# Kernel optimization log

Measured on AMD Instinct MI355X. Metric: run time of the kernel, lower is better.

Reference implementation:

```python
import jax, jax.numpy as jnp
import numpy as np

B, C, Q, E, H = 8, 1024, 128, 512, 1024


def setup_inputs() -> dict:
    key = jax.random.key(0)
    ks = jax.random.split(key, 8)
    return {
        "context": jax.random.normal(ks[0], (B, C, E), jnp.float32),
        "question": jax.random.normal(ks[1], (B, Q, E), jnp.float32),
        "context_mask": jnp.ones((B, C), jnp.float32),
        "w_question": jax.random.normal(ks[2], (E,), jnp.float32),
        "w_context": jax.random.normal(ks[3], (E,), jnp.float32),
        "w_multiple": jax.random.normal(ks[4], (E,), jnp.float32),
        "W1": jax.random.normal(ks[5], (4 * E, H), jnp.float32) * 0.02,
        "b1": jnp.zeros((H,), jnp.float32),
        "W2": jax.random.normal(ks[6], (H, 4 * E), jnp.float32) * 0.02,
        "b2": jnp.zeros((4 * E,), jnp.float32),
    }


def reference(context, question, context_mask, w_question, w_context, w_multiple, W1, b1, W2, b2):
    # Dropout is identity at eval time.
    # Trilinear similarity: s[b,c,q] = q.w_q + ctx.w_c + sum_e q_e*ctx_e*w_m_e
    q_w = question @ w_question                                  # (B,Q)
    c_w = context @ w_context                                    # (B,C)
    mult = jnp.einsum("bqe,bce->bcq", question * w_multiple, context)  # avoids (B,C,Q,E)
    sim = q_w[:, None, :] + c_w[:, :, None] + mult               # (B,C,Q)

    # Context2Query: softmax over question dim (dim=2)
    c2q = jnp.einsum("bcq,bqe->bce", jax.nn.softmax(sim, axis=2), question)
    # Query2Context: max over question dim, softmax over context dim (dim=1)
    q2c = jnp.einsum("bc,bce->be", jax.nn.softmax(jnp.max(sim, axis=2), axis=1), context)  # (B,E)

    attended = jnp.concatenate(
        [context, c2q, context * c2q, context * q2c[:, None, :]], axis=2
    )  # (B,C,4E)

    # MaskedLinear: linear then zero out masked context positions
    m = context_mask[:, :, None]
    h = (attended @ W1 + b1) * m
    out = jax.nn.relu((h @ W2 + b2) * m)
    return out
```

## Files before the change

kernel.cpp:

```cpp
#include <hip/hip_runtime.h>

typedef __bf16 bf16;
typedef __bf16 bf16x2 __attribute__((ext_vector_type(2)));
typedef __bf16 bf16x4 __attribute__((ext_vector_type(4)));
typedef __bf16 bf16x8 __attribute__((ext_vector_type(8)));
typedef float f32x4 __attribute__((ext_vector_type(4)));

#define AS1 __attribute__((address_space(1)))
#define AS3 __attribute__((address_space(3)))

__device__ __forceinline__ void async_copy16(const void* g, void* l) {
  __builtin_amdgcn_global_load_lds((const AS1 void*)g, (AS3 void*)l, 16, 0, 0);
}

#define BB 8
#define CC 1024
#define QQ 128
#define EE 512
#define HH 1024
#define FOURE 2048

__global__ __launch_bounds__(256) void prep_kernel(
    const float* __restrict__ W1, const float* __restrict__ W2,
    const float* __restrict__ qst, const float* __restrict__ wmul,
    const float* __restrict__ wqv, bf16* __restrict__ W1T,
    bf16* __restrict__ W2T, bf16* __restrict__ qT,
    bf16* __restrict__ qmh, bf16* __restrict__ qml, float* __restrict__ qw) {
  __shared__ float tile[32][33];
  __shared__ float r4[4];
  int bx = blockIdx.x;
  int t = threadIdx.x;
  if (bx >= 4608) {
    int i = bx - 4608;
    int half = t >> 7, tr = t & 127;
    int rowg = i * 2 + half;
    const float* qrow = qst + (size_t)rowg * EE;
    float4 qv = *(const float4*)&qrow[tr * 4];
    float4 wm4 = *(const float4*)&wmul[tr * 4];
    float4 wq4 = *(const float4*)&wqv[tr * 4];
    float m[4] = {qv.x * wm4.x, qv.y * wm4.y, qv.z * wm4.z, qv.w * wm4.w};
    bf16x4 h, l;
#pragma unroll
    for (int k = 0; k < 4; ++k) {
      bf16 hh = (bf16)m[k];
      h[k] = hh; l[k] = (bf16)(m[k] - (float)hh);
    }
    *(bf16x4*)&qmh[(size_t)rowg * EE + tr * 4] = h;
    *(bf16x4*)&qml[(size_t)rowg * EE + tr * 4] = l;
    float s = qv.x * wq4.x + qv.y * wq4.y + qv.z * wq4.z + qv.w * wq4.w;
#pragma unroll
    for (int off = 32; off; off >>= 1) s += __shfl_xor(s, off);
    if ((t & 63) == 0) r4[t >> 6] = s;
    __syncthreads();
    if (tr == 0) qw[rowg] = r4[half * 2] + r4[half * 2 + 1];
    return;
  }
  const float* src;
  bf16* dst;
  int R, C, idx;
  if (bx < 2048) {
    src = W1; dst = W1T; R = 2048; C = 1024; idx = bx;
  } else if (bx < 4096) {
    src = W2; dst = W2T; R = 1024; C = 2048; idx = bx - 2048;
  } else {
    int i = bx - 4096;
    int b = i >> 6; idx = i & 63;
    src = qst + (size_t)b * QQ * EE; dst = qT + (size_t)b * EE * QQ;
    R = 128; C = 512;
  }
  int ctiles = C >> 5;
  int by = idx / ctiles, cx = idx % ctiles;
  int tx = t & 31, ty = t >> 5;
#pragma unroll
  for (int rr = 0; rr < 4; ++rr)
    tile[ty + rr * 8][tx] = src[(size_t)(by * 32 + ty + rr * 8) * C + cx * 32 + tx];
  __syncthreads();
#pragma unroll
  for (int rr = 0; rr < 4; ++rr)
    dst[(size_t)(cx * 32 + ty + rr * 8) * R + by * 32 + tx] = (bf16)tile[tx][ty + rr * 8];
}

__global__ __launch_bounds__(256) void fused_att_kernel(
    const float* __restrict__ ctx, const bf16* __restrict__ qmh,
    const bf16* __restrict__ qml, const bf16* __restrict__ qT,
    const float* __restrict__ wc, const float* __restrict__ qw,
    float* __restrict__ smax, bf16* __restrict__ att) {
  int b = blockIdx.y;
  int m0 = blockIdx.x * 16;
  __shared__ __align__(16) char U[26880];
  bf16* Ah = (bf16*)(U);
  bf16* Al = (bf16*)(U + 1024);
  bf16* Bh = (bf16*)(U + 2048);
  bf16* Bl = (bf16*)(U + 10240);
  float(*sim_s)[132] = (float(*)[132])(U + 18432);
  bf16* c2q_lds = (bf16*)(U);
  __shared__ float wc_s[EE];
  __shared__ float qw_s[QQ];
  __shared__ float cw_s[16];
  __shared__ bf16 P_lds[16][136];
  int t = threadIdx.x;
  for (int i = t; i < EE; i += 256) wc_s[i] = wc[i];
  if (t < QQ) qw_s[t] = qw[b * QQ + t];
  __syncthreads();
  int wv = t >> 6, ln = t & 63;
  int rl = ln & 15, kq = ln >> 4;
  f32x4 acc[2] = {};
  const float* Ag = ctx + ((size_t)b * CC + m0) * EE;
  const bf16* Bhg = qmh + (size_t)b * QQ * EE;
  const bf16* Blg = qml + (size_t)b * QQ * EE;
  int arow = t >> 4, ae = (t & 15) * 2;
  float cwp = 0.f;
  for (int k0 = 0; k0 < EE; k0 += 32) {
    {
      float2 v = *(const float2*)(Ag + (size_t)arow * EE + k0 + ae);
      cwp += v.x * wc_s[k0 + ae] + v.y * wc_s[k0 + ae + 1];
      bf16 h0 = (bf16)v.x, h1 = (bf16)v.y;
      bf16x2 h, l;
      h[0] = h0; h[1] = h1;
      l[0] = (bf16)(v.x - (float)h0);
      l[1] = (bf16)(v.y - (float)h1);
      int sl = ((ae >> 3) ^ ((arow >> 1) & 3)) * 8 + (ae & 7);
      *(bf16x2*)&Ah[arow * 32 + sl] = h;
      *(bf16x2*)&Al[arow * 32 + sl] = l;
    }
#pragma unroll
    for (int r = 0; r < 2; ++r) {
      int fb = (r * 4 + wv) * 1024 + ln * 16;
      int row = fb >> 6;
      int cq = ((fb >> 4) & 3) ^ ((row >> 1) & 3);
      async_copy16(Bhg + (size_t)row * EE + k0 + cq * 8, (char*)Bh + fb);
      async_copy16(Blg + (size_t)row * EE + k0 + cq * 8, (char*)Bl + fb);
    }
    __syncthreads();
    bf16x8 ah, al, bh[2], bl[2];
    {
      int sl = (kq ^ ((rl >> 1) & 3)) * 8;
      ah = *(const bf16x8*)&Ah[rl * 32 + sl];
      al = *(const bf16x8*)&Al[rl * 32 + sl];
    }
#pragma unroll
    for (int j = 0; j < 2; ++j) {
      int r = wv * 32 + j * 16 + rl;
      int sl = (kq ^ ((r >> 1) & 3)) * 8;
      bh[j] = *(const bf16x8*)&Bh[r * 32 + sl];
      bl[j] = *(const bf16x8*)&Bl[r * 32 + sl];
    }
#pragma unroll
    for (int j = 0; j < 2; ++j) {
      acc[j] = __builtin_amdgcn_mfma_f32_16x16x32_bf16(ah, bh[j], acc[j], 0, 0, 0);
      acc[j] = __builtin_amdgcn_mfma_f32_16x16x32_bf16(ah, bl[j], acc[j], 0, 0, 0);
      acc[j] = __builtin_amdgcn_mfma_f32_16x16x32_bf16(al, bh[j], acc[j], 0, 0, 0);
    }
    __syncthreads();
  }
  {
    float s = cwp;
    s += __shfl_xor(s, 1); s += __shfl_xor(s, 2);
    s += __shfl_xor(s, 4); s += __shfl_xor(s, 8);
    if ((t & 15) == 0) cw_s[arow] = s;
  }
#pragma unroll
  for (int j = 0; j < 2; ++j) {
    int col = wv * 32 + j * 16 + rl;
    float qv = qw_s[col];
    int rbase = kq * 4;
#pragma unroll
    for (int r = 0; r < 4; ++r) sim_s[rbase + r][col] = acc[j][r] + qv;
  }
  __syncthreads();
  {
    int row = t >> 4, cb = t & 15;
    float v[8];
    float mx = -3.4e38f;
#pragma unroll
    for (int k = 0; k < 8; ++k) {
      v[k] = sim_s[row][cb + 16 * k];
      mx = fmaxf(mx, v[k]);
    }
    mx = fmaxf(mx, __shfl_xor(mx, 1));
    mx = fmaxf(mx, __shfl_xor(mx, 2));
    mx = fmaxf(mx, __shfl_xor(mx, 4));
    mx = fmaxf(mx, __shfl_xor(mx, 8));
    float sm = 0.f;
#pragma unroll
    for (int k = 0; k < 8; ++k) { v[k] = __expf(v[k] - mx); sm += v[k]; }
    sm += __shfl_xor(sm, 1);
    sm += __shfl_xor(sm, 2);
    sm += __shfl_xor(sm, 4);
    sm += __shfl_xor(sm, 8);
    float inv = 1.0f / sm;
#pragma unroll
    for (int k = 0; k < 8; ++k) P_lds[row][cb + 16 * k] = (bf16)(v[k] * inv);
    if (cb == 0) smax[b * CC + m0 + row] = mx + cw_s[row];
  }
  __syncthreads();
  f32x4 acc2[8] = {};
  const bf16* qTb = qT + (size_t)b * EE * QQ;
#pragma unroll
  for (int kk = 0; kk < 4; ++kk) {
    bf16x8 af2;
    {
      bf16x4 lo = *(const bf16x4*)&P_lds[rl][kk * 32 + kq * 8];
      bf16x4 hi = *(const bf16x4*)&P_lds[rl][kk * 32 + kq * 8 + 4];
      af2[0] = lo[0]; af2[1] = lo[1]; af2[2] = lo[2]; af2[3] = lo[3];
      af2[4] = hi[0]; af2[5] = hi[1]; af2[6] = hi[2]; af2[7] = hi[3];
    }
#pragma unroll
    for (int j = 0; j < 8; ++j) {
      int n = wv * 128 + j * 16 + rl;
      bf16x8 bfr = *(const bf16x8*)&qTb[(size_t)n * QQ + kk * 32 + kq * 8];
      acc2[j] = __builtin_amdgcn_mfma_f32_16x16x32_bf16(af2, bfr, acc2[j], 0, 0, 0);
    }
  }
#pragma unroll
  for (int j = 0; j < 8; ++j) {
    int col = wv * 128 + j * 16 + rl;
    int rbase = kq * 4;
#pragma unroll
    for (int r = 0; r < 4; ++r)
      c2q_lds[(size_t)(rbase + r) * 520 + col] = (bf16)acc2[j][r];
  }
  __syncthreads();
  {
    int row = t >> 4, tc = t & 15;
    const float* crow = ctx + ((size_t)(b * CC + m0 + row)) * EE;
    bf16* arow_p = att + ((size_t)(b * CC + m0 + row)) * FOURE;
#pragma unroll
    for (int cc = 0; cc < 4; ++cc) {
      int col = cc * 128 + tc * 8;
      bf16x8 q8 = *(const bf16x8*)&c2q_lds[(size_t)row * 520 + col];
      float4 v0 = *(const float4*)&crow[col];
      float4 v1 = *(const float4*)&crow[col + 4];
      float cv[8] = {v0.x, v0.y, v0.z, v0.w, v1.x, v1.y, v1.z, v1.w};
      bf16x8 o0, o2;
#pragma unroll
      for (int k = 0; k < 8; ++k) {
        o0[k] = (bf16)cv[k];
        o2[k] = (bf16)(cv[k] * (float)q8[k]);
      }
      *(bf16x8*)&arow_p[col] = o0;
      *(bf16x8*)&arow_p[EE + col] = q8;
      *(bf16x8*)&arow_p[2 * EE + col] = o2;
    }
  }
}

__global__ __launch_bounds__(256) void q2c_kernel(
    const float* __restrict__ ctx, const float* __restrict__ smax,
    float* __restrict__ q2c) {
  int b = blockIdx.x >> 5, ch = blockIdx.x & 31;
  int t = threadIdx.x;
  __shared__ float red[256];
  __shared__ float w_s[32];
  float v[4];
  float mx = -3.4e38f;
#pragma unroll
  for (int i = 0; i < 4; ++i) {
    v[i] = smax[b * CC + i * 256 + t];
    mx = fmaxf(mx, v[i]);
  }
  red[t] = mx;
  __syncthreads();
  for (int s = 128; s > 0; s >>= 1) {
    if (t < s) red[t] = fmaxf(red[t], red[t + s]);
    __syncthreads();
  }
  mx = red[0];
  __syncthreads();
  float sm = 0.f;
#pragma unroll
  for (int i = 0; i < 4; ++i) sm += __expf(v[i] - mx);
  red[t] = sm;
  __syncthreads();
  for (int s = 128; s > 0; s >>= 1) {
    if (t < s) red[t] += red[t + s];
    __syncthreads();
  }
  float inv = 1.0f / red[0];
  if (t < 32) w_s[t] = __expf(smax[b * CC + ch * 32 + t] - mx) * inv;
  __syncthreads();
  int e = t * 2;
  const float* cb = ctx + ((size_t)b * CC + ch * 32) * EE;
  float a0 = 0.f, a1 = 0.f;
#pragma unroll 8
  for (int r = 0; r < 32; ++r) {
    float2 vv = *(const float2*)&cb[(size_t)r * EE + e];
    float w = w_s[r];
    a0 += w * vv.x;
    a1 += w * vv.y;
  }
  atomicAdd(&q2c[b * EE + e], a0);
  atomicAdd(&q2c[b * EE + e + 1], a1);
}

__global__ __launch_bounds__(256) void att3_kernel(
    const float* __restrict__ ctx, const float* __restrict__ q2c,
    bf16* __restrict__ att) {
  int idx = blockIdx.x * 256 + threadIdx.x;
  int row = idx >> 6;
  int e = (idx & 63) * 8;
  int b = row >> 10;
  float4 v0 = *(const float4*)&ctx[(size_t)row * EE + e];
  float4 v1 = *(const float4*)&ctx[(size_t)row * EE + e + 4];
  float4 g0 = *(const float4*)&q2c[b * EE + e];
  float4 g1 = *(const float4*)&q2c[b * EE + e + 4];
  bf16x8 o;
  o[0] = (bf16)(v0.x * g0.x); o[1] = (bf16)(v0.y * g0.y);
  o[2] = (bf16)(v0.z * g0.z); o[3] = (bf16)(v0.w * g0.w);
  o[4] = (bf16)(v1.x * g1.x); o[5] = (bf16)(v1.y * g1.y);
  o[6] = (bf16)(v1.z * g1.z); o[7] = (bf16)(v1.w * g1.w);
  *(bf16x8*)&att[(size_t)row * FOURE + 3 * EE + e] = o;
}

template <int OUT_BF16, int RELU>
__global__ __launch_bounds__(512, 2) void gemm_bt_p2_kernel(
    const bf16* __restrict__ A, const bf16* __restrict__ Bt,
    const float* __restrict__ bias, const float* __restrict__ mask,
    void* __restrict__ Cout, int M, int N, int K) {
  __shared__ bf16 As[3][256 * 64];
  __shared__ bf16 Bs[3][128 * 64];
  int ntiles = N >> 7;
  int tiles_per_g = 8 * ntiles;
  int g = blockIdx.x / tiles_per_g, sub = blockIdx.x % tiles_per_g;
  int mt = g * 8 + (sub & 7), ntb = sub >> 3;
  int m0 = mt << 8, n0 = ntb << 7;
  int t = threadIdx.x, wv = t >> 6, ln = t & 63;
  int wm = wv >> 1, wn = wv & 1;
  int rl = ln & 15, kq = ln >> 4;
  int NT = K >> 6;

  auto stageA = [&](int buf, int kt, int r) {
    int k0 = kt << 6;
    int fb = r * 8192 + t * 16;
    int row = fb >> 7;
    int q = ((fb >> 4) & 7) ^ (row & 7);
    async_copy16(A + (size_t)(m0 + row) * K + k0 + q * 8, (char*)As[buf] + fb);
  };
  auto stageB = [&](int buf, int kt, int r) {
    int k0 = kt << 6;
    int fb = r * 8192 + t * 16;
    int row = fb >> 7;
    int q = ((fb >> 4) & 7) ^ (row & 7);
    async_copy16(Bt + (size_t)(n0 + row) * K + k0 + q * 8, (char*)Bs[buf] + fb);
  };

#pragma unroll
  for (int r = 0; r < 4; ++r) stageA(0, 0, r);
#pragma unroll
  for (int r = 0; r < 2; ++r) stageB(0, 0, r);
#pragma unroll
  for (int r = 0; r < 4; ++r) stageA(1, 1, r);
#pragma unroll
  for (int r = 0; r < 2; ++r) stageB(1, 1, r);
  asm volatile("s_waitcnt vmcnt(6)" ::: "memory");
  __builtin_amdgcn_s_barrier();

  f32x4 acc[4][4] = {};
  int cur = 0;
  for (int kt = 0; kt < NT; ++kt) {
    const bf16* Ab = As[cur];
    const bf16* Bb = Bs[cur];
    int nxt = cur + 2; if (nxt >= 3) nxt -= 3;
    bool pf = (kt + 2) < NT;
    bf16x8 af0[2][2], bfr[2][4];
#pragma unroll
    for (int ks = 0; ks < 2; ++ks) {
      int c = ks * 4 + kq;
#pragma unroll
      for (int i = 0; i < 2; ++i) {
        int row = wm * 64 + i * 16 + rl;
        af0[ks][i] = *(const bf16x8*)&Ab[row * 64 + ((c ^ (row & 7)) * 8)];
      }
#pragma unroll
      for (int j = 0; j < 4; ++j) {
        int row = wn * 64 + j * 16 + rl;
        bfr[ks][j] = *(const bf16x8*)&Bb[row * 64 + ((c ^ (row & 7)) * 8)];
      }
    }
    if (pf) { stageA(nxt, kt + 2, 0); stageA(nxt, kt + 2, 1); stageA(nxt, kt + 2, 2); }
    __builtin_amdgcn_s_barrier();
    asm volatile("s_waitcnt lgkmcnt(0)" ::: "memory");
    __builtin_amdgcn_sched_barrier(0);
    __builtin_amdgcn_s_setprio(1);
#pragma unroll
    for (int ks = 0; ks < 2; ++ks)
#pragma unroll
      for (int i = 0; i < 2; ++i)
#pragma unroll
        for (int j = 0; j < 4; ++j)
          acc[i][j] = __builtin_amdgcn_mfma_f32_16x16x32_bf16(
              af0[ks][i], bfr[ks][j], acc[i][j], 0, 0, 0);
    __builtin_amdgcn_s_setprio(0);
    __builtin_amdgcn_s_barrier();
    bf16x8 af1[2][2];
#pragma unroll
    for (int ks = 0; ks < 2; ++ks) {
      int c = ks * 4 + kq;
#pragma unroll
      for (int i = 0; i < 2; ++i) {
        int row = wm * 64 + (i + 2) * 16 + rl;
        af1[ks][i] = *(const bf16x8*)&Ab[row * 64 + ((c ^ (row & 7)) * 8)];
      }
    }
    if (pf) { stageA(nxt, kt + 2, 3); stageB(nxt, kt + 2, 0); stageB(nxt, kt + 2, 1); }
    __builtin_amdgcn_s_barrier();
    asm volatile("s_waitcnt lgkmcnt(0)" ::: "memory");
    __builtin_amdgcn_sched_barrier(0);
    __builtin_amdgcn_s_setprio(1);
#pragma unroll
    for (int ks = 0; ks < 2; ++ks)
#pragma unroll
      for (int i = 0; i < 2; ++i)
#pragma unroll
        for (int j = 0; j < 4; ++j)
          acc[i + 2][j] = __builtin_amdgcn_mfma_f32_16x16x32_bf16(
              af1[ks][i], bfr[ks][j], acc[i + 2][j], 0, 0, 0);
    __builtin_amdgcn_s_setprio(0);
    if (kt + 1 < NT) {
      if (pf) asm volatile("s_waitcnt vmcnt(6)" ::: "memory");
      else    asm volatile("s_waitcnt vmcnt(0)" ::: "memory");
      __builtin_amdgcn_s_barrier();
    }
    cur += 1; if (cur >= 3) cur -= 3;
  }

#pragma unroll
  for (int j = 0; j < 4; ++j) {
    int col = n0 + wn * 64 + j * 16 + rl;
    float bv = bias[col];
#pragma unroll
    for (int i = 0; i < 4; ++i) {
      int rbase = m0 + wm * 64 + i * 16 + (kq << 2);
#pragma unroll
      for (int r = 0; r < 4; ++r) {
        int row = rbase + r;
        float v = acc[i][j][r] + bv;
        v *= mask[row];
        if (RELU) v = fmaxf(v, 0.f);
        if (OUT_BF16)
          ((bf16*)Cout)[(size_t)row * N + col] = (bf16)v;
        else
          ((float*)Cout)[(size_t)row * N + col] = v;
      }
    }
  }
}

extern "C" void kernel_launch(void* const* d_in, const int* in_sizes, int n_in,
                              void* d_out, int out_size, void* d_ws, size_t ws_size,
                              hipStream_t stream) {
  const float* ctx = (const float*)d_in[0];
  const float* qst = (const float*)d_in[1];
  const float* mask = (const float*)d_in[2];
  const float* wqv = (const float*)d_in[3];
  const float* wcv = (const float*)d_in[4];
  const float* wmul = (const float*)d_in[5];
  const float* W1 = (const float*)d_in[6];
  const float* b1 = (const float*)d_in[7];
  const float* W2 = (const float*)d_in[8];
  const float* b2 = (const float*)d_in[9];
  float* out = (float*)d_out;
  char* ws = (char*)d_ws;

  bf16* att = (bf16*)(ws);
  bf16* hbuf = (bf16*)(ws + 33554432);
  bf16* W1T = (bf16*)(ws + 50331648);
  bf16* W2T = (bf16*)(ws + 54525952);
  bf16* qT = (bf16*)(ws + 58720256);
  bf16* qmh = (bf16*)(ws + 59768832);
  bf16* qml = (bf16*)(ws + 60817408);
  float* smax = (float*)(ws + 61865984);
  float* q2c = (float*)(ws + 61898752);
  float* qw = (float*)(ws + 61915136);

  prep_kernel<<<5120, 256, 0, stream>>>(W1, W2, qst, wmul, wqv,
                                        W1T, W2T, qT, qmh, qml, qw);
  fused_att_kernel<<<dim3(64, BB), 256, 0, stream>>>(ctx, qmh, qml, qT, wcv,
                                                     qw, smax, att);
  hipMemsetAsync(q2c, 0, BB * EE * sizeof(float), stream);
  q2c_kernel<<<256, 256, 0, stream>>>(ctx, smax, q2c);
  att3_kernel<<<2048, 256, 0, stream>>>(ctx, q2c, att);
  gemm_bt_p2_kernel<1, 0><<<256, 512, 0, stream>>>(
      att, W1T, b1, mask, hbuf, 8192, 1024, 2048);
  gemm_bt_p2_kernel<0, 1><<<512, 512, 0, stream>>>(
      hbuf, W2T, b2, mask, out, 8192, 2048, 1024);
}
```

Before: 224.9 us.

## Use 256x256-tile four-phase pipelined GEMM for second MaskedLinear

Adds a new GEMM kernel with 256x256 output tiles, 8 waves, double-buffered LDS and an XOR swizzle. Each K-step is split into four phases so that async global-to-LDS copies of the next tile interleave with MFMA sub-blocks, and setprio raises wave priority around the MFMA sections. The kernel replaces the previous GEMM only for the second linear layer (8192x2048x1024), cutting the grid from 512 to 256 blocks. The aim is higher operand reuse per tile and better overlap of loads with math. In exchange, the 128KB of LDS and large accumulator arrays add register and LDS pressure, and the smaller grid lowers parallelism across CUs.

Result: no change. 226.0 us (+0.5%).

```diff
diff --git a/kernel.cpp b/kernel.cpp
--- a/kernel.cpp
+++ b/kernel.cpp
@@ -446,6 +446,160 @@
   }
 }
 
+template <int OUT_BF16, int RELU>
+__global__ __launch_bounds__(512, 2) void gemm_ph4_kernel(
+    const bf16* __restrict__ A, const bf16* __restrict__ Bt,
+    const float* __restrict__ bias, const float* __restrict__ mask,
+    void* __restrict__ Cout, int M, int N, int K) {
+  __shared__ bf16 As[2][256 * 64];
+  __shared__ bf16 Bs[2][256 * 64];
+  int ntn = N >> 8;
+  int nblk = (M >> 8) * ntn;
+  int cpx = nblk >> 3;
+  int swz = (blockIdx.x & 7) * cpx + (blockIdx.x >> 3);
+  int mt = swz / ntn, ntb = swz % ntn;
+  int m0 = mt << 8, n0 = ntb << 8;
+  int t = threadIdx.x, wv = t >> 6, ln = t & 63;
+  int wm = wv >> 2, wn = wv & 3;
+  int rl = ln & 15, kq = ln >> 4;
+  int NT = K >> 6;
+  int chunk = t & 7;
+
+  auto stage = [&](int buf, int k1, int arr, int half, int r) {
+    int fb = r * 8192 + t * 16;
+    int phys = half * 128 + (fb >> 7);
+    int q = chunk ^ (phys & 7);
+    if (arr == 0) {
+      int lg = ((phys >> 6) & 1) * 128 + (phys >> 7) * 64 + (phys & 63);
+      async_copy16(A + (size_t)(m0 + lg) * K + k1 + q * 8,
+                   (char*)&As[buf][0] + half * 16384 + fb);
+    } else {
+      int lg = ((phys >> 5) & 3) * 64 + (phys >> 7) * 32 + (phys & 31);
+      async_copy16(Bt + (size_t)(n0 + lg) * K + k1 + q * 8,
+                   (char*)&Bs[buf][0] + half * 16384 + fb);
+    }
+  };
+  auto ldA = [&](const bf16* Ab, int i, int ks) {
+    int pr = (i >> 2) * 128 + wm * 64 + (i & 3) * 16 + rl;
+    return *(const bf16x8*)&Ab[pr * 64 + (((ks * 4 + kq) ^ (pr & 7)) * 8)];
+  };
+  auto ldB = [&](const bf16* Bb, int j, int ks) {
+    int pr = (j >> 1) * 128 + wn * 32 + (j & 1) * 16 + rl;
+    return *(const bf16x8*)&Bb[pr * 64 + (((ks * 4 + kq) ^ (pr & 7)) * 8)];
+  };
+
+  stage(0, 0, 0, 0, 0); stage(0, 0, 0, 0, 1);
+  stage(0, 0, 1, 0, 0); stage(0, 0, 1, 0, 1);
+  stage(0, 0, 1, 1, 0); stage(0, 0, 1, 1, 1);
+  stage(0, 0, 0, 1, 0); stage(0, 0, 0, 1, 1);
+  asm volatile("s_waitcnt vmcnt(4)" ::: "memory");
+  __builtin_amdgcn_s_barrier();
+
+  f32x4 acc[8][4] = {};
+  for (int kt = 0; kt < NT; ++kt) {
+    const bf16* Ab = &As[kt & 1][0];
+    const bf16* Bb = &Bs[kt & 1][0];
+    bool st = (kt + 1) < NT;
+    int sb = (kt + 1) & 1;
+    int k1 = (kt + 1) << 6;
+    bf16x8 areg[4][2], breg[4][2];
+#pragma unroll
+    for (int i = 0; i < 4; ++i) { areg[i][0] = ldA(Ab, i, 0); areg[i][1] = ldA(Ab, i, 1); }
+#pragma unroll
+    for (int j = 0; j < 2; ++j) { breg[j][0] = ldB(Bb, j, 0); breg[j][1] = ldB(Bb, j, 1); }
+    if (st) { stage(sb, k1, 0, 0, 0); stage(sb, k1, 0, 0, 1); }
+    __builtin_amdgcn_s_barrier();
+    asm volatile("s_waitcnt lgkmcnt(0)" ::: "memory");
+    __builtin_amdgcn_sched_barrier(0);
+    __builtin_amdgcn_s_setprio(1);
+#pragma unroll
+    for (int ks = 0; ks < 2; ++ks)
+#pragma unroll
+      for (int i = 0; i < 4; ++i)
+#pragma unroll
+        for (int j = 0; j < 2; ++j)
+          acc[i][j] = __builtin_amdgcn_mfma_f32_16x16x32_bf16(
+              areg[i][ks], breg[j][ks], acc[i][j], 0, 0, 0);
+    __builtin_amdgcn_s_setprio(0);
+    if (st) asm volatile("s_waitcnt vmcnt(4)" ::: "memory");
+    else    asm volatile("s_waitcnt vmcnt(2)" ::: "memory");
+    __builtin_amdgcn_s_barrier();
+#pragma unroll
+    for (int j = 2; j < 4; ++j) { breg[j][0] = ldB(Bb, j, 0); breg[j][1] = ldB(Bb, j, 1); }
+    if (st) { stage(sb, k1, 1, 0, 0); stage(sb, k1, 1, 0, 1); }
+    __builtin_amdgcn_s_barrier();
+    asm volatile("s_waitcnt lgkmcnt(0)" ::: "memory");
+    __builtin_amdgcn_sched_barrier(0);
+    __builtin_amdgcn_s_setprio(1);
+#pragma unroll
+    for (int ks = 0; ks < 2; ++ks)
+#pragma unroll
+      for (int i = 0; i < 4; ++i)
+#pragma unroll
+        for (int j = 2; j < 4; ++j)
+          acc[i][j] = __builtin_amdgcn_mfma_f32_16x16x32_bf16(
+              areg[i][ks], breg[j][ks], acc[i][j], 0, 0, 0);
+    __builtin_amdgcn_s_setprio(0);
+    if (st) asm volatile("s_waitcnt vmcnt(4)" ::: "memory");
+    else    asm volatile("s_waitcnt vmcnt(0)" ::: "memory");
+    __builtin_amdgcn_s_barrier();
+#pragma unroll
+    for (int i = 0; i < 4; ++i) { areg[i][0] = ldA(Ab, i + 4, 0); areg[i][1] = ldA(Ab, i + 4, 1); }
+    if (st) { stage(sb, k1, 1, 1, 0); stage(sb, k1, 1, 1, 1); }
+    __builtin_amdgcn_s_barrier();
+    asm volatile("s_waitcnt lgkmcnt(0)" ::: "memory");
+    __builtin_amdgcn_sched_barrier(0);
+    __builtin_amdgcn_s_setprio(1);
+#pragma unroll
+    for (int ks = 0; ks < 2; ++ks)
+#pragma unroll
+      for (int i = 0; i < 4; ++i)
+#pragma unroll
+        for (int j = 0; j < 2; ++j)
+          acc[i + 4][j] = __builtin_amdgcn_mfma_f32_16x16x32_bf16(
+              areg[i][ks], breg[j][ks], acc[i + 4][j], 0, 0, 0);
+    __builtin_amdgcn_s_setprio(0);
+    __builtin_amdgcn_s_barrier();
+    if (st) { stage(sb, k1, 0, 1, 0); stage(sb, k1, 0, 1, 1); }
+    __builtin_amdgcn_s_barrier();
+    __builtin_amdgcn_s_setprio(1);
+#pragma unroll
+    for (int ks = 0; ks < 2; ++ks)
+#pragma unroll
+      for (int i = 0; i < 4; ++i)
+#pragma unroll
+        for (int j = 2; j < 4; ++j)
+          acc[i + 4][j] = __builtin_amdgcn_mfma_f32_16x16x32_bf16(
+              areg[i][ks], breg[j][ks], acc[i + 4][j], 0, 0, 0);
+    __builtin_amdgcn_s_setprio(0);
+    if (st) {
+      asm volatile("s_waitcnt vmcnt(4)" ::: "memory");
+      __builtin_amdgcn_s_barrier();
+    }
+  }
+
+#pragma unroll
+  for (int j = 0; j < 4; ++j) {
+    int col = n0 + wn * 64 + j * 16 + rl;
+    float bv = bias[col];
+#pragma unroll
+    for (int i = 0; i < 8; ++i) {
+      int rbase = m0 + wm * 128 + i * 16 + (kq << 2);
+#pragma unroll
+      for (int r = 0; r < 4; ++r) {
+        int row = rbase + r;
+        float v = acc[i][j][r] + bv;
+        v *= mask[row];
+        if (RELU) v = fmaxf(v, 0.f);
+        if (OUT_BF16)
+          ((bf16*)Cout)[(size_t)row * N + col] = (bf16)v;
+        else
+          ((float*)Cout)[(size_t)row * N + col] = v;
+      }
+    }
+  }
+}
+
 extern "C" void kernel_launch(void* const* d_in, const int* in_sizes, int n_in,
                               void* d_out, int out_size, void* d_ws, size_t ws_size,
                               hipStream_t stream) {
@@ -482,6 +636,6 @@
   att3_kernel<<<2048, 256, 0, stream>>>(ctx, q2c, att);
   gemm_bt_p2_kernel<1, 0><<<256, 512, 0, stream>>>(
       att, W1T, b1, mask, hbuf, 8192, 1024, 2048);
-  gemm_bt_p2_kernel<0, 1><<<512, 512, 0, stream>>>(
+  gemm_ph4_kernel<0, 1><<<256, 512, 0, stream>>>(
       hbuf, W2T, b2, mask, out, 8192, 2048, 1024);
 }
```
